# Kernel optimization log

Measured on AMD Instinct MI355X. Metric: run time of the kernel, lower is better.

## Reference

```python
import jax, jax.numpy as jnp
import numpy as np
from jax import lax

B, L, D = 4, 4096, 1024
H = 4
DK = D // H   # head_k_dim = 256
DV = D // H   # head_v_dim = 256
HID = max(8, D // 2)  # gate trunk hidden = 512
CHUNK = 32
CONV_K = 4
EPS = 1e-5


def silu(x):
    return x * jax.nn.sigmoid(x)


def l2norm(x):
    return x * lax.rsqrt(jnp.sum(x * x, -1, keepdims=True) + 1e-6)


def causal_dwconv_silu(x, w):
    # x: (b,l,d), w: (d,k). Depthwise causal conv1d followed by SiLU (ShortConvolution).
    k = w.shape[-1]
    xp = jnp.pad(x, ((0, 0), (k - 1, 0), (0, 0))).transpose(0, 2, 1)  # (b,d,l+k-1)
    y = lax.conv_general_dilated(xp, w[:, None, :], (1,), 'VALID',
                                 feature_group_count=w.shape[0])
    return silu(y.transpose(0, 2, 1))


def delta_rule_chunkwise(q, k, v, beta, chunk=CHUNK):
    # q,k: (b,h,l,dk), v: (b,h,l,dv), beta: (b,h,l). l assumed multiple of chunk.
    b, h, l, dk = q.shape
    dv = v.shape[-1]
    n = l // chunk
    q = l2norm(q)
    k = l2norm(k)
    v = v * beta[..., None]
    kb = k * beta[..., None]
    qc = q.reshape(b, h, n, chunk, dk)
    kc = k.reshape(b, h, n, chunk, dk)
    vc = v.reshape(b, h, n, chunk, dv)
    kbc = kb.reshape(b, h, n, chunk, dk)
    # In-chunk triangular inverse: the torch loop computes (I + tril(kb k^T, -1))^{-1}
    Lm = jnp.tril(kbc @ jnp.swapaxes(kc, -1, -2), -1)  # strictly lower
    eye = jnp.eye(chunk, dtype=q.dtype)
    Tinv = jax.scipy.linalg.solve_triangular(eye + Lm, jnp.broadcast_to(eye, Lm.shape), lower=True)
    u = Tinv @ vc   # (b,h,n,c,dv)
    w = Tinv @ kbc  # (b,h,n,c,dk)
    strict = jnp.triu(jnp.ones((chunk, chunk), bool), 1)

    def step(S, inp):
        q_i, k_i, u_i, w_i = inp  # (b,h,c,d)
        attn = jnp.where(strict, 0.0, q_i @ jnp.swapaxes(k_i, -1, -2))
        u_hat = u_i - w_i @ S
        o_i = q_i @ S + attn @ u_hat
        return S + jnp.swapaxes(k_i, -1, -2) @ u_hat, o_i

    S0 = jnp.zeros((b, h, dk, dv), q.dtype)
    xs = tuple(jnp.moveaxis(t, 2, 0) for t in (qc, kc, u, w))
    S, o = lax.scan(step, S0, xs)
    o = jnp.moveaxis(o, 0, 2).reshape(b, h, l, dv)
    return o, S


def ema_rule(v, gamma):
    # v: (b,h,l,d), gamma: (b,h,l). Causal EMA: s_t = g_t*s_{t-1} + (1-g_t)*v_t
    def step(state, inp):
        v_t, g_t = inp
        state = g_t[..., None] * state + (1.0 - g_t[..., None]) * v_t
        return state, state

    s0 = jnp.zeros((v.shape[0], v.shape[1], v.shape[3]), v.dtype)
    _, out = lax.scan(step, s0, (jnp.moveaxis(v, 2, 0), jnp.moveaxis(gamma, 2, 0)))
    return jnp.moveaxis(out, 0, 2)


def hierarchical_gate(x, Wtrunk, btrunk, Wcoarse, bcoarse, Wlocal, blocal, Wglobal, bglobal, log_temp_c, log_temp_f):
    b, l, _ = x.shape
    z = silu(x @ Wtrunk.T + btrunk)  # (b,l,HID)
    tc = (jax.nn.softplus(log_temp_c) + 1e-4)[None, None, :, None]  # (1,1,h,1)
    tf = (jax.nn.softplus(log_temp_f) + 1e-4)[None, None, :, None]
    pg = jax.nn.softmax((z @ Wcoarse.T + bcoarse).reshape(b, l, H, 2) / tc, axis=-1)
    q = jax.nn.softmax((z @ Wlocal.T + blocal).reshape(b, l, H, 2) / tf, axis=-1)
    r = jax.nn.softmax((z @ Wglobal.T + bglobal).reshape(b, l, H, 2) / tf, axis=-1)
    w_v = pg[..., 0:1] * q[..., 0:1]
    w_es = pg[..., 0:1] * q[..., 1:2]
    w_d = pg[..., 1:2] * r[..., 0:1]
    w_el = pg[..., 1:2] * r[..., 1:2]
    return jnp.concatenate([w_v, w_es, w_d, w_el], axis=-1)  # (b,l,h,4)


def setup_inputs() -> dict:
    key = jax.random.key(0)
    ks = jax.random.split(key, 20)
    s = 0.02
    inp = {
        'hidden_states': jax.random.normal(ks[0], (B, L, D), jnp.float32),
        'Wq': jax.random.normal(ks[1], (D, D), jnp.float32) * s,
        'Wk': jax.random.normal(ks[2], (D, D), jnp.float32) * s,
        'Wv': jax.random.normal(ks[3], (D, D), jnp.float32) * s,
        'conv_q_w': jax.random.normal(ks[4], (D, CONV_K), jnp.float32) * 0.5,
        'conv_k_w': jax.random.normal(ks[5], (D, CONV_K), jnp.float32) * 0.5,
        'conv_v_w': jax.random.normal(ks[6], (D, CONV_K), jnp.float32) * 0.5,
        'Wb': jax.random.normal(ks[7], (H, D), jnp.float32) * s,
        'Wds': jax.random.normal(ks[8], (H, D), jnp.float32) * s,
        'bds': jnp.full((H,), -2.9444, jnp.float32),
        'Wdl': jax.random.normal(ks[9], (H, D), jnp.float32) * s,
        'bdl': jnp.full((H,), 2.9444, jnp.float32),
        'Wtrunk': jax.random.normal(ks[10], (HID, D), jnp.float32) * s,
        'btrunk': jnp.zeros((HID,), jnp.float32),
        'Wcoarse': jax.random.normal(ks[11], (H * 2, HID), jnp.float32) * s,
        'bcoarse': jnp.ones((H * 2,), jnp.float32),
        'Wlocal': jax.random.normal(ks[12], (H * 2, HID), jnp.float32) * s,
        'blocal': jnp.zeros((H * 2,), jnp.float32).at[::2].set(1.0),
        'Wglobal': jax.random.normal(ks[13], (H * 2, HID), jnp.float32) * s,
        'bglobal': jnp.zeros((H * 2,), jnp.float32).at[::2].set(1.0),
        'log_temp_c': jnp.zeros((H,), jnp.float32),  # log(1.0)
        'log_temp_f': jnp.zeros((H,), jnp.float32),
        'o_norm_w': jnp.ones((DV,), jnp.float32),
        'Wo': jax.random.normal(ks[14], (D, D), jnp.float32) * s,
    }
    return inp


def reference(hidden_states, Wq, Wk, Wv, conv_q_w, conv_k_w, conv_v_w, Wb, Wds, bds, Wdl, bdl,
              Wtrunk, btrunk, Wcoarse, bcoarse, Wlocal, blocal, Wglobal, bglobal,
              log_temp_c, log_temp_f, o_norm_w, Wo):
    x = hidden_states
    b, l, _ = x.shape
    # projections + short causal depthwise conv + SiLU
    q = causal_dwconv_silu(x @ Wq.T, conv_q_w).reshape(b, l, H, DK).transpose(0, 2, 1, 3)
    k = causal_dwconv_silu(x @ Wk.T, conv_k_w).reshape(b, l, H, DK).transpose(0, 2, 1, 3)
    v = causal_dwconv_silu(x @ Wv.T, conv_v_w).reshape(b, l, H, DV).transpose(0, 2, 1, 3)
    beta = jax.nn.sigmoid(x @ Wb.T).transpose(0, 2, 1)  # (b,h,l)
    delta_o, _ = delta_rule_chunkwise(q, k, v, beta)
    g_s = jax.nn.sigmoid(x @ Wds.T + bds).transpose(0, 2, 1)  # (b,h,l) short decay
    g_l = jax.nn.sigmoid(x @ Wdl.T + bdl).transpose(0, 2, 1)  # long decay
    ema_s = ema_rule(v, g_s)
    ema_l = ema_rule(v, g_l)
    weights = hierarchical_gate(x, Wtrunk, btrunk, Wcoarse, bcoarse, Wlocal, blocal,
                                Wglobal, bglobal, log_temp_c, log_temp_f)  # (b,l,h,4) [V,Es,D,El]
    v_b = v.transpose(0, 2, 1, 3)
    o = (weights[..., 0:1] * v_b
         + weights[..., 1:2] * ema_s.transpose(0, 2, 1, 3)
         + weights[..., 2:3] * delta_o.transpose(0, 2, 1, 3)
         + weights[..., 3:4] * ema_l.transpose(0, 2, 1, 3))
    # per-head RMSNorm
    o = o * lax.rsqrt(jnp.mean(o * o, -1, keepdims=True) + EPS) * o_norm_w
    return o.reshape(b, l, D) @ Wo.T
```

## Files before the change

### kernel.cpp

```cpp
#include <hip/hip_runtime.h>
#include <math.h>

#define BB 4
#define LL 4096
#define DD 1024
#define HH 4
#define DKk 256
#define DVv 256
#define HIDD 512
#define NC 128
#define NSEG 64
#define SEG 64

typedef unsigned short ushort_t;
typedef __attribute__((ext_vector_type(8))) short short8;
typedef __attribute__((ext_vector_type(4))) float floatx4;

__device__ __forceinline__ float sigm(float x) { return 1.f / (1.f + __expf(-x)); }

__device__ __forceinline__ float bf2f(ushort_t u) {
  union { unsigned int i; float f; } c; c.i = ((unsigned int)u) << 16; return c.f;
}
__device__ __forceinline__ ushort_t f2bf(float f) {
  union { float f; unsigned int i; } c; c.f = f;
  unsigned int lsb = (c.i >> 16) & 1u;
  return (ushort_t)((c.i + 0x7fffu + lsb) >> 16);
}
__device__ __forceinline__ void unpack2(unsigned int u, float& a, float& b) {
  union { unsigned int i; float f; } c0, c1;
  c0.i = u << 16; c1.i = u & 0xffff0000u; a = c0.f; b = c1.f;
}
__device__ __forceinline__ unsigned int pack2(float a, float b) {
  return (unsigned int)f2bf(a) | ((unsigned int)f2bf(b) << 16);
}
__device__ __forceinline__ void unpack8(const uint4 v, float* o) {
  unpack2(v.x, o[0], o[1]); unpack2(v.y, o[2], o[3]);
  unpack2(v.z, o[4], o[5]); unpack2(v.w, o[6], o[7]);
}
__device__ __forceinline__ float ubits(unsigned u) {
  union { unsigned i; float f; } c; c.i = u; return c.f;
}
__device__ __forceinline__ void split2t(float a, float b, unsigned& hi, unsigned& lo) {
  union { float f; unsigned u; } ca, cb; ca.f = a; cb.f = b;
  const unsigned ha = ca.u & 0xffff0000u, hb = cb.u & 0xffff0000u;
  hi = (ha >> 16) | hb;
  union { float f; unsigned u; } la, lb;
  la.f = a - ubits(ha); lb.f = b - ubits(hb);
  lo = (la.u >> 16) | (lb.u & 0xffff0000u);
}
__device__ __forceinline__ void gload16(const ushort_t* g, ushort_t* l) {
  __builtin_amdgcn_global_load_lds(
      (const __attribute__((address_space(1))) void*)g,
      (__attribute__((address_space(3))) void*)l, 16, 0, 0);
}

__global__ __launch_bounds__(256) void cvt_all_kernel(
    const float* __restrict__ x,  const float* __restrict__ Wq,
    const float* __restrict__ Wk, const float* __restrict__ Wv,
    const float* __restrict__ Wtr, const float* __restrict__ Wo,
    ushort_t* __restrict__ xb,  ushort_t* __restrict__ Wqb,
    ushort_t* __restrict__ Wkb, ushort_t* __restrict__ Wvb,
    ushort_t* __restrict__ Wtrb, ushort_t* __restrict__ Wob)
{
  const int NX = (int)((size_t)BB*LL*DD/8), NW = DD*DD/8, NT = HIDD*DD/8;
  int i = blockIdx.x * 256 + threadIdx.x;
  const float* src; ushort_t* dst;
  if (i < NX) { src = x; dst = xb; }
  else {
    i -= NX;
    if (i < NW) { src = Wq; dst = Wqb; }
    else { i -= NW;
      if (i < NW) { src = Wk; dst = Wkb; }
      else { i -= NW;
        if (i < NW) { src = Wv; dst = Wvb; }
        else { i -= NW;
          if (i < NT) { src = Wtr; dst = Wtrb; }
          else { i -= NT; if (i >= NW) return; src = Wo; dst = Wob; }
        }
      }
    }
  }
  const float4 a = ((const float4*)src)[2*i];
  const float4 b = ((const float4*)src)[2*i + 1];
  uint4 p;
  p.x = pack2(a.x, a.y); p.y = pack2(a.z, a.w);
  p.z = pack2(b.x, b.y); p.w = pack2(b.z, b.w);
  ((uint4*)dst)[i] = p;
}

template<int ACT, int BF16OUT>
__global__ __launch_bounds__(256) void gemm_bf16(const ushort_t* __restrict__ A,
    const ushort_t* __restrict__ W, const float* __restrict__ bias,
    void* __restrict__ Cv, int M, int N, int K)
{
  __shared__ ushort_t As[128*32];
  __shared__ ushort_t Ws[128*32];
  const int tid = threadIdx.x;
  const int bm = blockIdx.y * 128, bn = blockIdx.x * 128;
  const int lane = tid & 63, wave = tid >> 6;
  const int wm = (wave >> 1) * 64, wn = (wave & 1) * 64;
  const int fr = lane & 15, fq = lane >> 4;
  const int srow = wave * 16 + (lane >> 2);
  const int scol = (lane & 3) * 8;
  const ushort_t* Ap = A + (size_t)(bm + srow) * K + scol;
  const ushort_t* Wp = W + (size_t)(bn + srow) * K + scol;
  ushort_t* AsD = &As[wave * 512];
  ushort_t* WsD = &Ws[wave * 512];
  floatx4 acc[4][4];
#pragma unroll
  for (int i = 0; i < 4; ++i)
#pragma unroll
    for (int j = 0; j < 4; ++j) acc[i][j] = (floatx4){0.f, 0.f, 0.f, 0.f};

  for (int k0 = 0; k0 < K; k0 += 32) {
    __syncthreads();
    gload16(Ap + k0, AsD);
    gload16(Ap + (size_t)64 * K + k0, AsD + 64*32);
    gload16(Wp + k0, WsD);
    gload16(Wp + (size_t)64 * K + k0, WsD + 64*32);
    __syncthreads();
    short8 af[4], bf_[4];
#pragma unroll
    for (int mt = 0; mt < 4; ++mt)
      af[mt] = *(const short8*)&As[(wm + mt*16 + fr)*32 + fq*8];
#pragma unroll
    for (int nt = 0; nt < 4; ++nt)
      bf_[nt] = *(const short8*)&Ws[(wn + nt*16 + fr)*32 + fq*8];
#pragma unroll
    for (int mt = 0; mt < 4; ++mt)
#pragma unroll
      for (int nt = 0; nt < 4; ++nt)
        acc[mt][nt] = __builtin_amdgcn_mfma_f32_16x16x32_bf16(af[mt], bf_[nt], acc[mt][nt], 0, 0, 0);
  }
#pragma unroll
  for (int mt = 0; mt < 4; ++mt) {
#pragma unroll
    for (int reg = 0; reg < 4; ++reg) {
      const int row = bm + wm + mt*16 + fq*4 + reg;
#pragma unroll
      for (int nt = 0; nt < 4; ++nt) {
        const int col = bn + wn + nt*16 + fr;
        float v = acc[mt][nt][reg];
        if (ACT == 1) { v += bias[col]; v = v * sigm(v); }
        if (BF16OUT) ((ushort_t*)Cv)[(size_t)row * N + col] = f2bf(v);
        else         ((float*)Cv)[(size_t)row * N + col] = v;
      }
    }
  }
}

__global__ __launch_bounds__(256) void gemm_qkvt(const ushort_t* __restrict__ A,
    const ushort_t* __restrict__ Wcat, const float* __restrict__ btr,
    ushort_t* __restrict__ Cq, ushort_t* __restrict__ Ck,
    ushort_t* __restrict__ Cvv, ushort_t* __restrict__ Cz, int M, int K)
{
  __shared__ ushort_t As[128*32];
  __shared__ ushort_t Ws[128*32];
  const int tid = threadIdx.x;
  const int bm = blockIdx.y * 128, bn = blockIdx.x * 128;
  const int lane = tid & 63, wave = tid >> 6;
  const int wm = (wave >> 1) * 64, wn = (wave & 1) * 64;
  const int fr = lane & 15, fq = lane >> 4;
  const int srow = wave * 16 + (lane >> 2);
  const int scol = (lane & 3) * 8;
  const ushort_t* Ap = A + (size_t)(bm + srow) * K + scol;
  const ushort_t* Wp = Wcat + (size_t)(bn + srow) * K + scol;
  ushort_t* AsD = &As[wave * 512];
  ushort_t* WsD = &Ws[wave * 512];
  floatx4 acc[4][4];
#pragma unroll
  for (int i = 0; i < 4; ++i)
#pragma unroll
    for (int j = 0; j < 4; ++j) acc[i][j] = (floatx4){0.f, 0.f, 0.f, 0.f};

  for (int k0 = 0; k0 < K; k0 += 32) {
    __syncthreads();
    gload16(Ap + k0, AsD);
    gload16(Ap + (size_t)64 * K + k0, AsD + 64*32);
    gload16(Wp + k0, WsD);
    gload16(Wp + (size_t)64 * K + k0, WsD + 64*32);
    __syncthreads();
    short8 af[4], bf_[4];
#pragma unroll
    for (int mt = 0; mt < 4; ++mt)
      af[mt] = *(const short8*)&As[(wm + mt*16 + fr)*32 + fq*8];
#pragma unroll
    for (int nt = 0; nt < 4; ++nt)
      bf_[nt] = *(const short8*)&Ws[(wn + nt*16 + fr)*32 + fq*8];
#pragma unroll
    for (int mt = 0; mt < 4; ++mt)
#pragma unroll
      for (int nt = 0; nt < 4; ++nt)
        acc[mt][nt] = __builtin_amdgcn_mfma_f32_16x16x32_bf16(af[mt], bf_[nt], acc[mt][nt], 0, 0, 0);
  }
  const bool trunk = (bn >= 3072);
  ushort_t* dst;
  int nloc, cbase;
  if (!trunk) {
    const int mat = bn >> 10;
    dst = (mat == 0 ? Cq : (mat == 1 ? Ck : Cvv));
    nloc = 1024; cbase = bn & 1023;
  } else {
    dst = Cz; nloc = 512; cbase = bn - 3072;
  }
#pragma unroll
  for (int mt = 0; mt < 4; ++mt) {
#pragma unroll
    for (int reg = 0; reg < 4; ++reg) {
      const int row = bm + wm + mt*16 + fq*4 + reg;
#pragma unroll
      for (int nt = 0; nt < 4; ++nt) {
        const int col = cbase + wn + nt*16 + fr;
        float v = acc[mt][nt][reg];
        if (trunk) { v += btr[col]; v = v * sigm(v); }
        dst[(size_t)row * nloc + col] = f2bf(v);
      }
    }
  }
}

__global__ __launch_bounds__(256) void conv_silu_kernel(const ushort_t* __restrict__ xin,
    const float* __restrict__ wc, ushort_t* __restrict__ outp)
{
  const size_t i8 = (size_t)blockIdx.x * 256 + threadIdx.x;
  const int d8 = (int)((i8 & 127) << 3);
  const int l  = (int)((i8 >> 7) & (LL - 1));
  const int b  = (int)(i8 >> 19);
  const ushort_t* xp = xin + i8 * 8;
  const uint4 z4 = (uint4){0u,0u,0u,0u};
  const uint4 v0 = *(const uint4*)xp;
  const uint4 v1 = (l >= 1) ? *(const uint4*)(xp - DD)   : z4;
  const uint4 v2 = (l >= 2) ? *(const uint4*)(xp - 2*DD) : z4;
  const uint4 v3 = (l >= 3) ? *(const uint4*)(xp - 3*DD) : z4;
  float x0[8], x1[8], x2[8], x3[8];
  unpack8(v0, x0); unpack8(v1, x1); unpack8(v2, x2); unpack8(v3, x3);
  unsigned pk[4];
#pragma unroll
  for (int p = 0; p < 4; ++p) {
    float o2[2];
#pragma unroll
    for (int q = 0; q < 2; ++q) {
      const int j = p*2 + q;
      const float4 w = *(const float4*)(wc + (d8 + j) * 4);
      float acc = w.w * x0[j];
      acc = fmaf(w.z, x1[j], acc);
      acc = fmaf(w.y, x2[j], acc);
      acc = fmaf(w.x, x3[j], acc);
      o2[q] = acc * sigm(acc);
    }
    pk[p] = pack2(o2[0], o2[1]);
  }
  const int h = d8 >> 8, dk = d8 & 255;
  *(uint4*)(outp + (((size_t)(b*HH + h))*LL + l)*DKk + dk) = *(uint4*)pk;
}

__global__ __launch_bounds__(256) void small_proj_kernel(const float* __restrict__ x,
   const float* __restrict__ Wb, const float* __restrict__ Wds, const float* __restrict__ bds,
   const float* __restrict__ Wdl, const float* __restrict__ bdl,
   float* __restrict__ beta, float* __restrict__ gs, float* __restrict__ gl)
{
  const int bl = blockIdx.x;
  const int t = threadIdx.x, wave = t >> 6, lane = t & 63;
  __shared__ float res[12];
  const float* xr = x + (size_t)bl * DD + lane * 16;
  const float4 x0 = *(const float4*)(xr);
  const float4 x1 = *(const float4*)(xr + 4);
  const float4 x2 = *(const float4*)(xr + 8);
  const float4 x3 = *(const float4*)(xr + 12);
  for (int rr = 0; rr < 3; ++rr) {
    const int r = wave * 3 + rr;
    const int mat = r >> 2, h = r & 3;
    const float* Wr = (mat == 0 ? Wb : (mat == 1 ? Wds : Wdl)) + (size_t)h * DD + lane * 16;
    const float4 w0 = *(const float4*)(Wr);
    const float4 w1 = *(const float4*)(Wr + 4);
    const float4 w2 = *(const float4*)(Wr + 8);
    const float4 w3 = *(const float4*)(Wr + 12);
    float p = x0.x*w0.x + x0.y*w0.y + x0.z*w0.z + x0.w*w0.w
            + x1.x*w1.x + x1.y*w1.y + x1.z*w1.z + x1.w*w1.w
            + x2.x*w2.x + x2.y*w2.y + x2.z*w2.z + x2.w*w2.w
            + x3.x*w3.x + x3.y*w3.y + x3.z*w3.z + x3.w*w3.w;
#pragma unroll
    for (int o = 1; o < 64; o <<= 1) p += __shfl_xor(p, o);
    if (lane == 0) res[r] = p;
  }
  __syncthreads();
  if (t < 12) {
    const int mat = t >> 2, h = t & 3;
    float v = res[t];
    if (mat == 1) v += bds[h];
    if (mat == 2) v += bdl[h];
    v = sigm(v);
    const int b = bl >> 12, l = bl & (LL - 1);
    const size_t o = ((size_t)(b*HH + h))*LL + l;
    (mat == 0 ? beta : (mat == 1 ? gs : gl))[o] = v;
  }
}

__global__ __launch_bounds__(256) void gate_kernel(const ushort_t* __restrict__ z,
  const float* __restrict__ Wc, const float* __restrict__ bc,
  const float* __restrict__ Wl, const float* __restrict__ bl_,
  const float* __restrict__ Wg, const float* __restrict__ bg,
  const float* __restrict__ ltc, const float* __restrict__ ltf,
  float* __restrict__ wgt)
{
  const int bl = blockIdx.x;
  const int t = threadIdx.x, wave = t >> 6, lane = t & 63;
  __shared__ float res[24];
  const uint4 zv = *(const uint4*)(z + (size_t)bl * HIDD + lane * 8);
  float zf[8]; unpack8(zv, zf);
  for (int rr = 0; rr < 6; ++rr) {
    const int r = wave * 6 + rr;
    const int mat = r >> 3, qi = r & 7;
    const float* Wr = (mat == 0 ? Wc : (mat == 1 ? Wl : Wg)) + (size_t)qi * HIDD + lane * 8;
    const float4 w0 = *(const float4*)(Wr);
    const float4 w1 = *(const float4*)(Wr + 4);
    float p = zf[0]*w0.x + zf[1]*w0.y + zf[2]*w0.z + zf[3]*w0.w
            + zf[4]*w1.x + zf[5]*w1.y + zf[6]*w1.z + zf[7]*w1.w;
#pragma unroll
    for (int o = 1; o < 64; o <<= 1) p += __shfl_xor(p, o);
    if (lane == 0) {
      const float* br = (mat == 0 ? bc : (mat == 1 ? bl_ : bg));
      res[r] = p + br[qi];
    }
  }
  __syncthreads();
  if (t < 4) {
    const float tc = logf(1.f + __expf(ltc[t])) + 1e-4f;
    const float tf = logf(1.f + __expf(ltf[t])) + 1e-4f;
    const float pg0 = sigm((res[2*t]     - res[2*t+1])     / tc);
    const float q0  = sigm((res[8+2*t]   - res[8+2*t+1])   / tf);
    const float r0  = sigm((res[16+2*t]  - res[16+2*t+1])  / tf);
    float* o = wgt + ((size_t)bl * HH + t) * 4;
    o[0] = pg0 * q0;         o[1] = pg0 * (1.f - q0);
    o[2] = (1.f - pg0) * r0; o[3] = (1.f - pg0) * (1.f - r0);
  }
}

#define QS 264
__global__ __launch_bounds__(256) void prep_kernel(ushort_t* __restrict__ q,
    ushort_t* __restrict__ k, const ushort_t* __restrict__ v,
    const float* __restrict__ beta,
    ushort_t* __restrict__ u, ushort_t* __restrict__ w,
    ushort_t* __restrict__ ah, ushort_t* __restrict__ al)
{
  __shared__ ushort_t qb[32*QS];
  __shared__ ushort_t kb[32*QS];
  __shared__ float Lm[32*32];
  __shared__ float betas[32];
  const int bid = blockIdx.x;
  const int ci = bid & (NC - 1);
  const int bh = bid >> 7;
  const int t = threadIdx.x;
  const size_t base = ((size_t)bh * LL + ci*32) * DKk;
  if (t < 32) betas[t] = beta[(size_t)bh * LL + ci*32 + t];
  for (int i4 = t; i4 < 1024; i4 += 256) {
    const int r = i4 >> 5, e = (i4 & 31) * 8;
    *(uint4*)&qb[r*QS + e] = *(const uint4*)(q + base + r*256 + e);
    *(uint4*)&kb[r*QS + e] = *(const uint4*)(k + base + r*256 + e);
  }
  __syncthreads();
  {
    const int r = t >> 3, g = t & 7;
    const int e0 = g * 32;
    float qf[32], kf[32];
#pragma unroll
    for (int j = 0; j < 4; ++j) {
      const uint4 qv = *(const uint4*)&qb[r*QS + e0 + j*8];
      const uint4 kv = *(const uint4*)&kb[r*QS + e0 + j*8];
      unpack8(qv, qf + j*8); unpack8(kv, kf + j*8);
    }
    float sq = 0.f, sk = 0.f;
#pragma unroll
    for (int j = 0; j < 32; ++j) {
      sq = fmaf(qf[j], qf[j], sq);
      sk = fmaf(kf[j], kf[j], sk);
    }
#pragma unroll
    for (int o = 1; o < 8; o <<= 1) { sq += __shfl_xor(sq, o); sk += __shfl_xor(sk, o); }
    const float rq = rsqrtf(sq + 1e-6f), rk = rsqrtf(sk + 1e-6f);
#pragma unroll
    for (int j = 0; j < 4; ++j) {
      uint4 qo, ko;
      qo.x = pack2(qf[j*8+0]*rq, qf[j*8+1]*rq);
      qo.y = pack2(qf[j*8+2]*rq, qf[j*8+3]*rq);
      qo.z = pack2(qf[j*8+4]*rq, qf[j*8+5]*rq);
      qo.w = pack2(qf[j*8+6]*rq, qf[j*8+7]*rq);
      ko.x = pack2(kf[j*8+0]*rk, kf[j*8+1]*rk);
      ko.y = pack2(kf[j*8+2]*rk, kf[j*8+3]*rk);
      ko.z = pack2(kf[j*8+4]*rk, kf[j*8+5]*rk);
      ko.w = pack2(kf[j*8+6]*rk, kf[j*8+7]*rk);
      *(uint4*)&qb[r*QS + e0 + j*8] = qo;
      *(uint4*)&kb[r*QS + e0 + j*8] = ko;
    }
  }
  __syncthreads();
  for (int i4 = t; i4 < 1024; i4 += 256) {
    const int r = i4 >> 5, e = (i4 & 31) * 8;
    *(uint4*)(q + base + r*256 + e) = *(const uint4*)&qb[r*QS + e];
  }
  {
    unsigned int pk[16];
#pragma unroll
    for (int j = 0; j < 16; ++j)
      pk[j] = (unsigned int)kb[(2*j)*QS + t] | ((unsigned int)kb[(2*j+1)*QS + t] << 16);
    uint4* kd = (uint4*)(k + base + (size_t)t*32);
#pragma unroll
    for (int j = 0; j < 4; ++j) kd[j] = ((const uint4*)pk)[j];
  }
  {
    const int lane = t & 63, wv4 = t >> 6;
    const int fr = lane & 15, fq = lane >> 4;
    const int it = wv4 >> 1, jt = wv4 & 1;
    floatx4 dq = (floatx4){0.f,0.f,0.f,0.f};
    floatx4 dk2 = (floatx4){0.f,0.f,0.f,0.f};
#pragma unroll
    for (int ks = 0; ks < 8; ++ks) {
      const short8 bfk = *(const short8*)&kb[(jt*16+fr)*QS + ks*32 + fq*8];
      const short8 afq = *(const short8*)&qb[(it*16+fr)*QS + ks*32 + fq*8];
      const short8 afk = *(const short8*)&kb[(it*16+fr)*QS + ks*32 + fq*8];
      dq  = __builtin_amdgcn_mfma_f32_16x16x32_bf16(afq, bfk, dq, 0,0,0);
      dk2 = __builtin_amdgcn_mfma_f32_16x16x32_bf16(afk, bfk, dk2, 0,0,0);
    }
#pragma unroll
    for (int reg = 0; reg < 4; ++reg) {
      const int i = it*16 + fq*4 + reg;
      const int j = jt*16 + fr;
      const float av = (j <= i) ? dq[reg] : 0.f;
      const ushort_t hh = f2bf(av);
      const size_t aoff = ((size_t)bh*NC + ci)*1024 + (size_t)i*32 + j;
      ah[aoff] = hh;
      al[aoff] = f2bf(av - bf2f(hh));
      Lm[i*32 + j] = (j < i) ? betas[i] * dk2[reg] : 0.f;
    }
  }
  __syncthreads();
  {
    float cu[32], cw[32];
#pragma unroll
    for (int r = 0; r < 32; ++r) {
      cu[r] = bf2f(v[base + r*256 + t]) * betas[r];
      cw[r] = bf2f(kb[r*QS + t]) * betas[r];
    }
#pragma unroll
    for (int i = 1; i < 32; ++i) {
      float au = cu[i], aw = cw[i];
#pragma unroll
      for (int jb = 0; jb < (i + 3) / 4; ++jb) {
        const float4 lr = *(const float4*)&Lm[i*32 + jb*4];
        const float lmv[4] = {lr.x, lr.y, lr.z, lr.w};
#pragma unroll
        for (int qv = 0; qv < 4; ++qv) {
          const int j = jb*4 + qv;
          if (j < i) {
            au = fmaf(-lmv[qv], cu[j], au);
            aw = fmaf(-lmv[qv], cw[j], aw);
          }
        }
      }
      cu[i] = au; cw[i] = aw;
    }
    {
      unsigned int pu[16];
#pragma unroll
      for (int j = 0; j < 16; ++j) pu[j] = pack2(cu[2*j], cu[2*j+1]);
      uint4* ud = (uint4*)(u + base + (size_t)t*32);
#pragma unroll
      for (int j = 0; j < 4; ++j) ud[j] = ((const uint4*)pu)[j];
    }
#pragma unroll
    for (int r = 0; r < 32; ++r) w[base + r*256 + t] = f2bf(cw[r]);
  }
}

#define S16(dv,kk) (((dv)<<8) + ((kk) ^ (((dv)&7)<<3)))
#define U16(dv,cr) (((dv)<<5) + ((cr) ^ (((dv)&3)<<3)))

struct FragsK { short8 kf[4]; short8 afh, afl; };
struct FragsA { short8 aw[8]; uint2 uu; };

__global__ __launch_bounds__(256, 1) void scan_kernel(
    const ushort_t* __restrict__ qn, const ushort_t* __restrict__ kt,
    const ushort_t* __restrict__ ut, const ushort_t* __restrict__ w,
    const ushort_t* __restrict__ ah, const ushort_t* __restrict__ al,
    float* __restrict__ dout)
{
  __shared__ ushort_t STh[16*256];
  __shared__ ushort_t STl[16*256];
  __shared__ ushort_t Uh[16*32];
  __shared__ ushort_t Ul[16*32];
  const int bid = blockIdx.x;
  const int bh = bid & 15, vs = bid >> 4;
  const int b = bh >> 2, h = bh & 3;
  const int t = threadIdx.x, lane = t & 63, wv = t >> 6;
  const int fr = lane & 15, fq = lane >> 4;
  const int mt = wv & 1;
  const bool isW = (wv < 2);

  for (int i = t; i < 512; i += 256) {
    ((uint4*)STh)[i] = (uint4){0u,0u,0u,0u};
    ((uint4*)STl)[i] = (uint4){0u,0u,0u,0u};
  }

  const size_t bhL = (size_t)bh * LL;
  const ushort_t* wqB = (isW ? w : qn) + bhL * DKk;
  const ushort_t* kB  = kt + bhL * DKk;
  const ushort_t* uB  = ut + bhL * DVv;
  const ushort_t* ahB = ah + (size_t)bh * NC * 1024;
  const ushort_t* alB = al + (size_t)bh * NC * 1024;
  float* oB = dout + (size_t)b * LL * DD + h * DVv + vs * 16 + fr;

  floatx4 Sacc[4];
#pragma unroll
  for (int i = 0; i < 4; ++i) Sacc[i] = (floatx4){0.f,0.f,0.f,0.f};

  auto loadK = [&](int ci, FragsK& f) {
    const ushort_t* kp = kB + (size_t)ci*8192 + (size_t)(wv*64 + fr)*32 + fq*8;
#pragma unroll
    for (int m = 0; m < 4; ++m) f.kf[m] = *(const short8*)(kp + m*512);
    if (!isW) {
      f.afh = *(const short8*)(ahB + (size_t)ci*1024 + (mt*16+fr)*32 + fq*8);
      f.afl = *(const short8*)(alB + (size_t)ci*1024 + (mt*16+fr)*32 + fq*8);
    }
  };
  auto loadA = [&](int ci, FragsA& f) {
    const ushort_t* ap = wqB + (size_t)(ci*32 + mt*16 + fr) * DKk + fq*8;
#pragma unroll
    for (int ks = 0; ks < 8; ++ks) f.aw[ks] = *(const short8*)(ap + ks*32);
    if (isW)
      f.uu = *(const uint2*)(uB + (size_t)ci*8192 + (size_t)(vs*16 + fr)*32 + mt*16 + fq*4);
  };

  FragsK k0, k1; FragsA a0, a1;
  loadK(0, k0);
  loadA(0, a0);
  __syncthreads();

  auto body = [&](int ci, FragsK& kc, FragsK& kn, FragsA& ac, FragsA& an) {
    if (ci + 1 < NC) { loadK(ci + 1, kn); loadA(ci + 1, an); }
    floatx4 acc0, acc1;
    if (isW) {
      float u0,u1,u2,u3; unpack2(ac.uu.x,u0,u1); unpack2(ac.uu.y,u2,u3);
      acc0 = (floatx4){-u0,-u1,-u2,-u3};
      acc1 = (floatx4){0.f,0.f,0.f,0.f};
#pragma unroll
      for (int ks = 0; ks < 8; ++ks) {
        const short8 sh = *(const short8*)&STh[S16(fr, ks*32 + fq*8)];
        const short8 sl = *(const short8*)&STl[S16(fr, ks*32 + fq*8)];
        acc0 = __builtin_amdgcn_mfma_f32_16x16x32_bf16(ac.aw[ks], sh, acc0, 0,0,0);
        acc1 = __builtin_amdgcn_mfma_f32_16x16x32_bf16(ac.aw[ks], sl, acc1, 0,0,0);
      }
      const float v0 = -(acc0[0]+acc1[0]), v1 = -(acc0[1]+acc1[1]);
      const float v2 = -(acc0[2]+acc1[2]), v3 = -(acc0[3]+acc1[3]);
      unsigned ph0, pl0, ph1, pl1;
      split2t(v0, v1, ph0, pl0); split2t(v2, v3, ph1, pl1);
      *(uint2*)&Uh[U16(fr, mt*16 + fq*4)] = (uint2){ph0, ph1};
      *(uint2*)&Ul[U16(fr, mt*16 + fq*4)] = (uint2){pl0, pl1};
    } else {
      acc0 = (floatx4){0.f,0.f,0.f,0.f};
#pragma unroll
      for (int ks = 0; ks < 8; ++ks) {
        const short8 sh = *(const short8*)&STh[S16(fr, ks*32 + fq*8)];
        acc0 = __builtin_amdgcn_mfma_f32_16x16x32_bf16(ac.aw[ks], sh, acc0, 0,0,0);
      }
    }
    __syncthreads();
    const short8 uhh = *(const short8*)&Uh[U16(fr, fq*8)];
    const short8 uhl = *(const short8*)&Ul[U16(fr, fq*8)];
    if (!isW) {
      acc0 = __builtin_amdgcn_mfma_f32_16x16x32_bf16(kc.afh, uhh, acc0, 0,0,0);
      acc0 = __builtin_amdgcn_mfma_f32_16x16x32_bf16(kc.afh, uhl, acc0, 0,0,0);
      acc0 = __builtin_amdgcn_mfma_f32_16x16x32_bf16(kc.afl, uhh, acc0, 0,0,0);
      float* op = oB + (size_t)(ci*32 + mt*16 + fq*4) * DD;
#pragma unroll
      for (int r = 0; r < 4; ++r) op[(size_t)r * DD] = acc0[r];
    }
#pragma unroll
    for (int m = 0; m < 4; ++m) {
      Sacc[m] = __builtin_amdgcn_mfma_f32_16x16x32_bf16(kc.kf[m], uhh, Sacc[m], 0,0,0);
      Sacc[m] = __builtin_amdgcn_mfma_f32_16x16x32_bf16(kc.kf[m], uhl, Sacc[m], 0,0,0);
    }
#pragma unroll
    for (int m = 0; m < 4; ++m) {
      unsigned ph0, pl0, ph1, pl1;
      split2t(Sacc[m][0], Sacc[m][1], ph0, pl0);
      split2t(Sacc[m][2], Sacc[m][3], ph1, pl1);
      const int dk0 = wv*64 + m*16 + fq*4;
      *(uint2*)&STh[S16(fr, dk0)] = (uint2){ph0, ph1};
      *(uint2*)&STl[S16(fr, dk0)] = (uint2){pl0, pl1};
    }
    __syncthreads();
  };

  for (int c2 = 0; c2 < NC; c2 += 2) {
    body(c2,     k0, k1, a0, a1);
    body(c2 + 1, k1, k0, a1, a0);
  }
}

__global__ __launch_bounds__(256) void ema_local_kernel(const ushort_t* __restrict__ v,
  const float* __restrict__ gs, const float* __restrict__ gl,
  ushort_t* __restrict__ es, ushort_t* __restrict__ el,
  float* __restrict__ Bs, float* __restrict__ Bl,
  float* __restrict__ As, float* __restrict__ Al,
  float* __restrict__ PfS, float* __restrict__ PfL)
{
  const int bid = blockIdx.x;
  const int seg = bid & (NSEG - 1), bh = bid >> 6;
  const int b = bh >> 2, h = bh & 3;
  const int dv = threadIdx.x;
  const int l0 = seg * SEG;
  const ushort_t* vp = v + ((size_t)bh*LL + l0) * DVv + dv;
  const float* gsp = gs + (size_t)bh*LL + l0;
  const float* glp = gl + (size_t)bh*LL + l0;
  ushort_t* esp = es + ((size_t)b*LL + l0)*DD + h*DVv + dv;
  ushort_t* elp = el + ((size_t)b*LL + l0)*DD + h*DVv + dv;
  float* pfs = PfS + (size_t)bh*LL + l0;
  float* pfl = PfL + (size_t)bh*LL + l0;
  float s1 = 0.f, s2 = 0.f, p1 = 1.f, p2 = 1.f;
  for (int j = 0; j < SEG; ++j) {
    const float vv = bf2f(vp[(size_t)j * DVv]);
    const float a = gsp[j], g2 = glp[j];
    s1 = fmaf(a,  s1, (1.f - a)  * vv);
    s2 = fmaf(g2, s2, (1.f - g2) * vv);
    p1 *= a; p2 *= g2;
    esp[(size_t)j * DD] = f2bf(s1);
    elp[(size_t)j * DD] = f2bf(s2);
    if (dv == 0) { pfs[j] = p1; pfl[j] = p2; }
  }
  const size_t o = (((size_t)bh*NSEG + seg) << 8) + dv;
  Bs[o] = s1; Bl[o] = s2;
  if (dv == 0) { As[bh*NSEG + seg] = p1; Al[bh*NSEG + seg] = p2; }
}

__global__ __launch_bounds__(256) void ema_carry_kernel(
  const float* __restrict__ Bs, const float* __restrict__ Bl,
  const float* __restrict__ As, const float* __restrict__ Al,
  float* __restrict__ Cs, float* __restrict__ Cl)
{
  const int bh = blockIdx.x;
  const int dv = threadIdx.x;
  __shared__ float Ash[NSEG], Alh[NSEG];
  if (dv < NSEG) { Ash[dv] = As[bh*NSEG + dv]; Alh[dv] = Al[bh*NSEG + dv]; }
  __syncthreads();
  float c1 = 0.f, c2 = 0.f;
  for (int s = 0; s < NSEG; ++s) {
    const size_t o = (((size_t)bh*NSEG + s) << 8) + dv;
    Cs[o] = c1; Cl[o] = c2;
    c1 = fmaf(Ash[s], c1, Bs[o]);
    c2 = fmaf(Alh[s], c2, Bl[o]);
  }
}

__global__ __launch_bounds__(256) void combine_kernel(const ushort_t* __restrict__ v,
  const ushort_t* __restrict__ es, const ushort_t* __restrict__ el,
  const float* __restrict__ dov, const float* __restrict__ wgt,
  const float* __restrict__ onw,
  const float* __restrict__ Cs, const float* __restrict__ Cl,
  const float* __restrict__ PfS, const float* __restrict__ PfL,
  ushort_t* __restrict__ outp)
{
  const int bid = blockIdx.x * 4 + (threadIdx.x >> 6);
  const int h = bid & 3;
  const size_t bl = (size_t)(bid >> 2);
  const int lane = threadIdx.x & 63;
  const size_t b = bl >> 12;
  const size_t l = bl & (LL - 1);
  const int bh = (int)(b * HH) + h;
  const int seg = (int)(l >> 6);
  const size_t vidx = (((b*HH + h) * (size_t)LL) + l) * DVv + lane*4;
  const size_t didx = bl * DD + h*DVv + lane*4;
  const uint2 vu = *(const uint2*)(v + vidx);
  const uint2 eu = *(const uint2*)(es + didx);
  const uint2 gu = *(const uint2*)(el + didx);
  const float4 d4 = *(const float4*)(dov + didx);
  const float pS = PfS[(size_t)bh*LL + l];
  const float pL = PfL[(size_t)bh*LL + l];
  const float4 cs4 = *(const float4*)(Cs + (((size_t)bh*NSEG + seg) << 8) + lane*4);
  const float4 cl4 = *(const float4*)(Cl + (((size_t)bh*NSEG + seg) << 8) + lane*4);
  float vf[4], ef[4], gf[4];
  unpack2(vu.x, vf[0], vf[1]); unpack2(vu.y, vf[2], vf[3]);
  unpack2(eu.x, ef[0], ef[1]); unpack2(eu.y, ef[2], ef[3]);
  unpack2(gu.x, gf[0], gf[1]); unpack2(gu.y, gf[2], gf[3]);
  ef[0] = fmaf(pS, cs4.x, ef[0]); ef[1] = fmaf(pS, cs4.y, ef[1]);
  ef[2] = fmaf(pS, cs4.z, ef[2]); ef[3] = fmaf(pS, cs4.w, ef[3]);
  gf[0] = fmaf(pL, cl4.x, gf[0]); gf[1] = fmaf(pL, cl4.y, gf[1]);
  gf[2] = fmaf(pL, cl4.z, gf[2]); gf[3] = fmaf(pL, cl4.w, gf[3]);
  const float* wp = wgt + (size_t)bid * 4;
  const float w0 = wp[0], w1 = wp[1], w2 = wp[2], w3 = wp[3];
  float o[4];
  const float df[4] = {d4.x, d4.y, d4.z, d4.w};
  float ss = 0.f;
#pragma unroll
  for (int i = 0; i < 4; ++i) {
    o[i] = w0*vf[i] + w1*ef[i] + w2*df[i] + w3*gf[i];
    ss = fmaf(o[i], o[i], ss);
  }
#pragma unroll
  for (int off = 1; off < 64; off <<= 1) ss += __shfl_xor(ss, off);
  const float sc = rsqrtf(ss * (1.f / DVv) + 1e-5f);
  const float4 nw = *(const float4*)(onw + lane*4);
  uint2 pk;
  pk.x = pack2(o[0]*sc*nw.x, o[1]*sc*nw.y);
  pk.y = pack2(o[2]*sc*nw.z, o[3]*sc*nw.w);
  *(uint2*)(outp + didx) = pk;
}

extern "C" void kernel_launch(void* const* d_in, const int* in_sizes, int n_in,
                              void* d_out, int out_size, void* d_ws, size_t ws_size,
                              hipStream_t stream)
{
  const float* x    = (const float*)d_in[0];
  const float* Wq   = (const float*)d_in[1];
  const float* Wk   = (const float*)d_in[2];
  const float* Wv   = (const float*)d_in[3];
  const float* cqw  = (const float*)d_in[4];
  const float* ckw  = (const float*)d_in[5];
  const float* cvw  = (const float*)d_in[6];
  const float* Wb   = (const float*)d_in[7];
  const float* Wds  = (const float*)d_in[8];
  const float* bds  = (const float*)d_in[9];
  const float* Wdl  = (const float*)d_in[10];
  const float* bdl  = (const float*)d_in[11];
  const float* Wtr  = (const float*)d_in[12];
  const float* btr  = (const float*)d_in[13];
  const float* Wc   = (const float*)d_in[14];
  const float* bc   = (const float*)d_in[15];
  const float* Wl   = (const float*)d_in[16];
  const float* blc  = (const float*)d_in[17];
  const float* Wg   = (const float*)d_in[18];
  const float* bg   = (const float*)d_in[19];
  const float* ltc  = (const float*)d_in[20];
  const float* ltf  = (const float*)d_in[21];
  const float* onw  = (const float*)d_in[22];
  const float* Wo   = (const float*)d_in[23];
  float* outp = (float*)d_out;

  const size_t BLD = (size_t)BB * LL * DD;
  unsigned char* w8 = (unsigned char*)d_ws;
  const size_t SL = BLD * 2;
  ushort_t* SA = (ushort_t*)(w8 + 0*SL);
  ushort_t* SB = (ushort_t*)(w8 + 1*SL);
  ushort_t* SC = (ushort_t*)(w8 + 2*SL);
  ushort_t* SD = (ushort_t*)(w8 + 3*SL);
  ushort_t* SE = (ushort_t*)(w8 + 4*SL);
  ushort_t* zb   = (ushort_t*)(w8 + 5*SL);
  ushort_t* attn_hi = (ushort_t*)(w8 + 5*SL + BLD);
  ushort_t* attn_lo = attn_hi + (size_t)BB*HH*NC*1024;
  float*    beta = (float*)(attn_hi + 2*(size_t)BB*HH*NC*1024);
  float*    gs   = beta + (size_t)BB*HH*LL;
  float*    gl   = gs   + (size_t)BB*HH*LL;
  float*    wgt  = gl   + (size_t)BB*HH*LL;
  float*    Bs   = wgt  + (size_t)BB*LL*HH*4;
  float*    Bl   = Bs   + (size_t)BB*HH*NSEG*256;
  float*    Cs   = Bl   + (size_t)BB*HH*NSEG*256;
  float*    Cl   = Cs   + (size_t)BB*HH*NSEG*256;
  float*    As   = Cl   + (size_t)BB*HH*NSEG*256;
  float*    Al   = As   + (size_t)BB*HH*NSEG;
  float*    PfS  = Al   + (size_t)BB*HH*NSEG;
  float*    PfL  = PfS  + (size_t)BB*HH*LL;
  ushort_t* Wqb  = (ushort_t*)(PfL + (size_t)BB*HH*LL);
  ushort_t* Wkb  = Wqb + (size_t)DD*DD;
  ushort_t* Wvb  = Wkb + (size_t)DD*DD;
  ushort_t* Wtrb = Wvb + (size_t)DD*DD;
  ushort_t* Wob  = Wtrb + (size_t)HIDD*DD;
  ushort_t* xb   = SD;
  float*    dov  = outp;

  const int MBL = BB * LL;
  dim3 blk256(256);

  {
    const int NTOT = (int)(BLD/8) + 4*(DD*DD/8) + HIDD*DD/8;
    cvt_all_kernel<<<dim3((NTOT + 255)/256), blk256, 0, stream>>>(
        x, Wq, Wk, Wv, Wtr, Wo, xb, Wqb, Wkb, Wvb, Wtrb, Wob);
  }

  gemm_qkvt<<<dim3(28, MBL/128), blk256, 0, stream>>>(xb, Wqb, btr, SA, SB, SC, zb, MBL, DD);
  small_proj_kernel<<<dim3(MBL), blk256, 0, stream>>>(x, Wb, Wds, bds, Wdl, bdl, beta, gs, gl);
  gate_kernel<<<dim3(MBL), blk256, 0, stream>>>(zb, Wc, bc, Wl, blc, Wg, bg, ltc, ltf, wgt);
  conv_silu_kernel<<<dim3((unsigned)(BLD/8/256)), blk256, 0, stream>>>(SA, cqw, SD);
  conv_silu_kernel<<<dim3((unsigned)(BLD/8/256)), blk256, 0, stream>>>(SB, ckw, SA);
  conv_silu_kernel<<<dim3((unsigned)(BLD/8/256)), blk256, 0, stream>>>(SC, cvw, SB);
  prep_kernel<<<dim3(BB*HH*NC), blk256, 0, stream>>>(SD, SA, SB, beta, SC, SE, attn_hi, attn_lo);
  scan_kernel<<<dim3(256), blk256, 0, stream>>>(SD, SA, SC, SE, attn_hi, attn_lo, dov);
  ema_local_kernel<<<dim3(BB*HH*NSEG), blk256, 0, stream>>>(SB, gs, gl, SE, SD, Bs, Bl, As, Al, PfS, PfL);
  ema_carry_kernel<<<dim3(BB*HH), blk256, 0, stream>>>(Bs, Bl, As, Al, Cs, Cl);
  combine_kernel<<<dim3(MBL*HH/4), blk256, 0, stream>>>(SB, SE, SD, dov, wgt, onw, Cs, Cl, PfS, PfL, SA);
  gemm_bf16<0,0><<<dim3(DD/128, MBL/128), blk256, 0, stream>>>(SA, Wob, nullptr, outp, MBL, DD, DD);
}
```

Baseline: 1.016 ms.

## Remap GEMM blocks per XCD, store delta output as bf16, widen scan LDS swizzle

```diff
diff --git a/kernel.cpp b/kernel.cpp
--- a/kernel.cpp
+++ b/kernel.cpp
@@ -88,15 +88,20 @@
   ((uint4*)dst)[i] = p;
 }
 
-template<int ACT, int BF16OUT>
+template<int BF16OUT>
 __global__ __launch_bounds__(256) void gemm_bf16(const ushort_t* __restrict__ A,
-    const ushort_t* __restrict__ W, const float* __restrict__ bias,
-    void* __restrict__ Cv, int M, int N, int K)
+    const ushort_t* __restrict__ W, void* __restrict__ Cv, int M, int N, int K)
 {
   __shared__ ushort_t As[128*32];
   __shared__ ushort_t Ws[128*32];
+  const int bid = blockIdx.x;
+  const int xcd = bid & 7;
+  const int idx = bid >> 3;
+  const int xB = idx >> 4;
+  const int yl = idx & 15;
+  const int yB = xcd + (yl << 3);
   const int tid = threadIdx.x;
-  const int bm = blockIdx.y * 128, bn = blockIdx.x * 128;
+  const int bm = yB * 128, bn = xB * 128;
   const int lane = tid & 63, wave = tid >> 6;
   const int wm = (wave >> 1) * 64, wn = (wave & 1) * 64;
   const int fr = lane & 15, fq = lane >> 4;
@@ -140,8 +145,7 @@
 #pragma unroll
       for (int nt = 0; nt < 4; ++nt) {
         const int col = bn + wn + nt*16 + fr;
-        float v = acc[mt][nt][reg];
-        if (ACT == 1) { v += bias[col]; v = v * sigm(v); }
+        const float v = acc[mt][nt][reg];
         if (BF16OUT) ((ushort_t*)Cv)[(size_t)row * N + col] = f2bf(v);
         else         ((float*)Cv)[(size_t)row * N + col] = v;
       }
@@ -156,8 +160,14 @@
 {
   __shared__ ushort_t As[128*32];
   __shared__ ushort_t Ws[128*32];
+  const int bid = blockIdx.x;
+  const int xcd = bid & 7;
+  const int idx = bid >> 3;
+  const int xB = idx >> 4;
+  const int yl = idx & 15;
+  const int yB = xcd + (yl << 3);
   const int tid = threadIdx.x;
-  const int bm = blockIdx.y * 128, bn = blockIdx.x * 128;
+  const int bm = yB * 128, bn = xB * 128;
   const int lane = tid & 63, wave = tid >> 6;
   const int wm = (wave >> 1) * 64, wn = (wave & 1) * 64;
   const int fr = lane & 15, fq = lane >> 4;
@@ -472,7 +482,7 @@
   }
 }
 
-#define S16(dv,kk) (((dv)<<8) + ((kk) ^ (((dv)&7)<<3)))
+#define S16(dv,kk) (((dv)<<8) + ((kk) ^ (((dv)&15)<<3)))
 #define U16(dv,cr) (((dv)<<5) + ((cr) ^ (((dv)&3)<<3)))
 
 struct FragsK { short8 kf[4]; short8 afh, afl; };
@@ -482,7 +492,7 @@
     const ushort_t* __restrict__ qn, const ushort_t* __restrict__ kt,
     const ushort_t* __restrict__ ut, const ushort_t* __restrict__ w,
     const ushort_t* __restrict__ ah, const ushort_t* __restrict__ al,
-    float* __restrict__ dout)
+    ushort_t* __restrict__ dout)
 {
   __shared__ ushort_t STh[16*256];
   __shared__ ushort_t STl[16*256];
@@ -507,7 +517,7 @@
   const ushort_t* uB  = ut + bhL * DVv;
   const ushort_t* ahB = ah + (size_t)bh * NC * 1024;
   const ushort_t* alB = al + (size_t)bh * NC * 1024;
-  float* oB = dout + (size_t)b * LL * DD + h * DVv + vs * 16 + fr;
+  ushort_t* oB = dout + (size_t)b * LL * DD + h * DVv + vs * 16 + fr;
 
   floatx4 Sacc[4];
 #pragma unroll
@@ -570,9 +580,9 @@
       acc0 = __builtin_amdgcn_mfma_f32_16x16x32_bf16(kc.afh, uhh, acc0, 0,0,0);
       acc0 = __builtin_amdgcn_mfma_f32_16x16x32_bf16(kc.afh, uhl, acc0, 0,0,0);
       acc0 = __builtin_amdgcn_mfma_f32_16x16x32_bf16(kc.afl, uhh, acc0, 0,0,0);
-      float* op = oB + (size_t)(ci*32 + mt*16 + fq*4) * DD;
-#pragma unroll
-      for (int r = 0; r < 4; ++r) op[(size_t)r * DD] = acc0[r];
+      ushort_t* op = oB + (size_t)(ci*32 + mt*16 + fq*4) * DD;
+#pragma unroll
+      for (int r = 0; r < 4; ++r) op[(size_t)r * DD] = f2bf(acc0[r]);
     }
 #pragma unroll
     for (int m = 0; m < 4; ++m) {
@@ -653,7 +663,7 @@
 
 __global__ __launch_bounds__(256) void combine_kernel(const ushort_t* __restrict__ v,
   const ushort_t* __restrict__ es, const ushort_t* __restrict__ el,
-  const float* __restrict__ dov, const float* __restrict__ wgt,
+  const ushort_t* __restrict__ dovb, const float* __restrict__ wgt,
   const float* __restrict__ onw,
   const float* __restrict__ Cs, const float* __restrict__ Cl,
   const float* __restrict__ PfS, const float* __restrict__ PfL,
@@ -672,15 +682,16 @@
   const uint2 vu = *(const uint2*)(v + vidx);
   const uint2 eu = *(const uint2*)(es + didx);
   const uint2 gu = *(const uint2*)(el + didx);
-  const float4 d4 = *(const float4*)(dov + didx);
+  const uint2 du = *(const uint2*)(dovb + didx);
   const float pS = PfS[(size_t)bh*LL + l];
   const float pL = PfL[(size_t)bh*LL + l];
   const float4 cs4 = *(const float4*)(Cs + (((size_t)bh*NSEG + seg) << 8) + lane*4);
   const float4 cl4 = *(const float4*)(Cl + (((size_t)bh*NSEG + seg) << 8) + lane*4);
-  float vf[4], ef[4], gf[4];
+  float vf[4], ef[4], gf[4], df[4];
   unpack2(vu.x, vf[0], vf[1]); unpack2(vu.y, vf[2], vf[3]);
   unpack2(eu.x, ef[0], ef[1]); unpack2(eu.y, ef[2], ef[3]);
   unpack2(gu.x, gf[0], gf[1]); unpack2(gu.y, gf[2], gf[3]);
+  unpack2(du.x, df[0], df[1]); unpack2(du.y, df[2], df[3]);
   ef[0] = fmaf(pS, cs4.x, ef[0]); ef[1] = fmaf(pS, cs4.y, ef[1]);
   ef[2] = fmaf(pS, cs4.z, ef[2]); ef[3] = fmaf(pS, cs4.w, ef[3]);
   gf[0] = fmaf(pL, cl4.x, gf[0]); gf[1] = fmaf(pL, cl4.y, gf[1]);
@@ -688,7 +699,6 @@
   const float* wp = wgt + (size_t)bid * 4;
   const float w0 = wp[0], w1 = wp[1], w2 = wp[2], w3 = wp[3];
   float o[4];
-  const float df[4] = {d4.x, d4.y, d4.z, d4.w};
   float ss = 0.f;
 #pragma unroll
   for (int i = 0; i < 4; ++i) {
@@ -764,7 +774,7 @@
   ushort_t* Wtrb = Wvb + (size_t)DD*DD;
   ushort_t* Wob  = Wtrb + (size_t)HIDD*DD;
   ushort_t* xb   = SD;
-  float*    dov  = outp;
+  ushort_t* dovb = (ushort_t*)outp;
 
   const int MBL = BB * LL;
   dim3 blk256(256);
@@ -775,16 +785,16 @@
         x, Wq, Wk, Wv, Wtr, Wo, xb, Wqb, Wkb, Wvb, Wtrb, Wob);
   }
 
-  gemm_qkvt<<<dim3(28, MBL/128), blk256, 0, stream>>>(xb, Wqb, btr, SA, SB, SC, zb, MBL, DD);
+  gemm_qkvt<<<dim3(28*128), blk256, 0, stream>>>(xb, Wqb, btr, SA, SB, SC, zb, MBL, DD);
   small_proj_kernel<<<dim3(MBL), blk256, 0, stream>>>(x, Wb, Wds, bds, Wdl, bdl, beta, gs, gl);
   gate_kernel<<<dim3(MBL), blk256, 0, stream>>>(zb, Wc, bc, Wl, blc, Wg, bg, ltc, ltf, wgt);
   conv_silu_kernel<<<dim3((unsigned)(BLD/8/256)), blk256, 0, stream>>>(SA, cqw, SD);
   conv_silu_kernel<<<dim3((unsigned)(BLD/8/256)), blk256, 0, stream>>>(SB, ckw, SA);
   conv_silu_kernel<<<dim3((unsigned)(BLD/8/256)), blk256, 0, stream>>>(SC, cvw, SB);
   prep_kernel<<<dim3(BB*HH*NC), blk256, 0, stream>>>(SD, SA, SB, beta, SC, SE, attn_hi, attn_lo);
-  scan_kernel<<<dim3(256), blk256, 0, stream>>>(SD, SA, SC, SE, attn_hi, attn_lo, dov);
+  scan_kernel<<<dim3(256), blk256, 0, stream>>>(SD, SA, SC, SE, attn_hi, attn_lo, dovb);
   ema_local_kernel<<<dim3(BB*HH*NSEG), blk256, 0, stream>>>(SB, gs, gl, SE, SD, Bs, Bl, As, Al, PfS, PfL);
   ema_carry_kernel<<<dim3(BB*HH), blk256, 0, stream>>>(Bs, Bl, As, Al, Cs, Cl);
-  combine_kernel<<<dim3(MBL*HH/4), blk256, 0, stream>>>(SB, SE, SD, dov, wgt, onw, Cs, Cl, PfS, PfL, SA);
-  gemm_bf16<0,0><<<dim3(DD/128, MBL/128), blk256, 0, stream>>>(SA, Wob, nullptr, outp, MBL, DD, DD);
-}
+  combine_kernel<<<dim3(MBL*HH/4), blk256, 0, stream>>>(SB, SE, SD, dovb, wgt, onw, Cs, Cl, PfS, PfL, SA);
+  gemm_bf16<0><<<dim3(8*128), blk256, 0, stream>>>(SA, Wob, outp, MBL, DD, DD);
+}
```

Result: no change. 1.001 ms (-1.5%).
